# Optimization experiments

Hardware: AMD Instinct MI355X
Metric: run time of the kernel (lower is better)

Reference implementation:

```python
import jax, jax.numpy as jnp
import numpy as np

G_DATA = 262144   # full-resolution grid nodes
G_TRUNC = 40000   # truncated grid nodes
E_EDGES = 1048576 # edges per direction (~4 per data node)
FEAT = 128
EPS = 1e-8


def _sparse_project(x, src, dst, w, dst_size):
    """Row-normalized sparse projection: y[d] = sum_e w_e x[src_e] / sum_e w_e.

    x: [N, G_src, F] -> [N, dst_size, F]
    """
    msg = x[:, src, :] * w[None, :, None]              # [N, E, F] gather-multiply
    out = jnp.zeros((x.shape[0], dst_size, x.shape[2]), dtype=x.dtype)
    out = out.at[:, dst, :].add(msg)                    # scatter-add over dst
    norm = jnp.zeros((dst_size,), dtype=x.dtype).at[dst].add(w)
    return out / jnp.maximum(norm, EPS)[None, :, None]


def setup_inputs() -> dict:
    key = jax.random.key(0)
    ks = jax.random.split(key, 7)
    x = jax.random.normal(ks[0], (1, 2, 1, G_DATA, FEAT), dtype=jnp.float32)
    down_src = jax.random.randint(ks[1], (E_EDGES,), 0, G_DATA, dtype=jnp.int32)
    down_dst = jax.random.randint(ks[2], (E_EDGES,), 0, G_TRUNC, dtype=jnp.int32)
    down_w = jax.random.uniform(ks[3], (E_EDGES,), dtype=jnp.float32)
    up_src = jax.random.randint(ks[4], (E_EDGES,), 0, G_TRUNC, dtype=jnp.int32)
    up_dst = jax.random.randint(ks[5], (E_EDGES,), 0, G_DATA, dtype=jnp.int32)
    up_w = jax.random.uniform(ks[6], (E_EDGES,), dtype=jnp.float32)
    return {"x": x, "down_src": down_src, "down_dst": down_dst, "down_w": down_w,
            "up_src": up_src, "up_dst": up_dst, "up_w": up_w}


def reference(x, down_src, down_dst, down_w, up_src, up_dst, up_w):
    batch = x.shape[0]
    xt = x[:, -1, ...]                                   # [B, E, G, F] take last time step
    b, e, g, f = xt.shape
    xt = xt.reshape(b * e, g, f)                         # (batch ensemble) grid features
    xc = _sparse_project(xt, down_src, down_dst, down_w, G_TRUNC)   # down-project
    xr = _sparse_project(xc, up_src, up_dst, up_w, G_DATA)          # up-project
    return xr.reshape(batch, e, g, f)
```

## Files before the change

kernel.cpp:

```cpp
#include <hip/hip_runtime.h>

#define G_DATA 262144
#define G_TRUNC 40000
#define E_EDGES 1048576
#define FEAT 128
#define EPS 1e-8f


__global__ __launch_bounds__(256) void hist_kernel(const int* __restrict__ dst,
                                                   int* __restrict__ counts) {
    int e = blockIdx.x * 256 + threadIdx.x;
    if (e < E_EDGES) atomicAdd(&counts[dst[e]], 1);
}

__global__ __launch_bounds__(1024) void scan_block(const int* __restrict__ counts,
                                                   int rows,
                                                   int* __restrict__ off,
                                                   int* __restrict__ bsums) {
    __shared__ int s[1024];
    int tid = threadIdx.x;
    int idx = blockIdx.x * 1024 + tid;
    int c = (idx < rows) ? counts[idx] : 0;
    s[tid] = c;
    for (int d = 1; d < 1024; d <<= 1) {
        __syncthreads();
        int t = (tid >= d) ? s[tid - d] : 0;
        __syncthreads();
        s[tid] += t;
    }
    if (idx < rows) off[idx] = s[tid] - c;
    if (tid == 1023) bsums[blockIdx.x] = s[1023];
}

__global__ __launch_bounds__(256) void scan_bsums(int* __restrict__ bsums, int n) {
    __shared__ int s[256];
    int tid = threadIdx.x;
    int v = (tid < n) ? bsums[tid] : 0;
    s[tid] = v;
    for (int d = 1; d < 256; d <<= 1) {
        __syncthreads();
        int t = (tid >= d) ? s[tid - d] : 0;
        __syncthreads();
        s[tid] += t;
    }
    if (tid < n) bsums[tid] = s[tid] - v;
}

__global__ __launch_bounds__(256) void finalize_off(int* __restrict__ off,
                                                    const int* __restrict__ bsums,
                                                    int* __restrict__ cursor,
                                                    int rows, int total) {
    int idx = blockIdx.x * 256 + threadIdx.x;
    if (idx < rows) {
        int o = off[idx] + bsums[idx >> 10];
        off[idx] = o;
        cursor[idx] = o;
    }
    if (idx == 0) off[rows] = total;
}

__global__ __launch_bounds__(256) void scatter_pairs(const int* __restrict__ src,
                                                     const int* __restrict__ dst,
                                                     const float* __restrict__ w,
                                                     int* __restrict__ cursor,
                                                     int2* __restrict__ pairs) {
    int e = blockIdx.x * 256 + threadIdx.x;
    if (e >= E_EDGES) return;
    int d = dst[e];
    int pos = atomicAdd(&cursor[d], 1);
    pairs[pos] = make_int2(src[e], __float_as_int(w[e]));
}

__global__ __launch_bounds__(256) void gather_rows(const float* __restrict__ xsrc,
                                                   const int2* __restrict__ pairs,
                                                   const int* __restrict__ off,
                                                   float* __restrict__ out,
                                                   int rows) {
    long gid = (long)blockIdx.x * 256 + threadIdx.x;
    int r    = (int)(gid >> 6);
    int lane = (int)(gid & 63);
    if (r >= rows) return;
    int beg = off[r], end = off[r + 1];
    float ax = 0.f, ay = 0.f, wsum = 0.f;
    for (int k = beg; k < end; ++k) {
        int2 p = pairs[k];
        float ww = __int_as_float(p.y);
        float2 v = ((const float2*)(xsrc + (size_t)p.x * FEAT))[lane];
        ax += ww * v.x;
        ay += ww * v.y;
        wsum += ww;
    }
    float den = fmaxf(wsum, EPS);
    float2 o;
    o.x = ax / den;
    o.y = ay / den;
    ((float2*)(out + (size_t)r * FEAT))[lane] = o;
}


__global__ __launch_bounds__(256) void norm_accum(const int* __restrict__ dst,
                                                  const float* __restrict__ w,
                                                  float* __restrict__ norm) {
    int i = blockIdx.x * blockDim.x + threadIdx.x;
    if (i < E_EDGES) atomicAdd(&norm[dst[i]], w[i]);
}

__global__ __launch_bounds__(256) void scatter_accum(const float* __restrict__ xsrc,
                                                     const int* __restrict__ src,
                                                     const int* __restrict__ dst,
                                                     const float* __restrict__ w,
                                                     float* __restrict__ out) {
    long gid = (long)blockIdx.x * blockDim.x + threadIdx.x;
    int e    = (int)(gid >> 6);
    int lane = (int)(gid & 63);
    if (e >= E_EDGES) return;
    int   s  = src[e];
    int   d  = dst[e];
    float ww = w[e];
    float2 v = ((const float2*)(xsrc + (size_t)s * FEAT))[lane];
    float* op = out + (size_t)d * FEAT + lane * 2;
    atomicAdd(op,     v.x * ww);
    atomicAdd(op + 1, v.y * ww);
}

__global__ __launch_bounds__(256) void row_divide(float* __restrict__ data,
                                                  const float* __restrict__ norm,
                                                  int rows) {
    long gid = (long)blockIdx.x * blockDim.x + threadIdx.x;
    int r = (int)(gid >> 5);
    int c = (int)(gid & 31);
    if (r >= rows) return;
    float den = fmaxf(norm[r], EPS);
    float4* p = (float4*)(data + (size_t)r * FEAT) + c;
    float4 v = *p;
    v.x /= den; v.y /= den; v.z /= den; v.w /= den;
    *p = v;
}


extern "C" void kernel_launch(void* const* d_in, const int* in_sizes, int n_in,
                              void* d_out, int out_size, void* d_ws, size_t ws_size,
                              hipStream_t stream) {
    const float* x        = (const float*)d_in[0];
    const int*   down_src = (const int*)  d_in[1];
    const int*   down_dst = (const int*)  d_in[2];
    const float* down_w   = (const float*)d_in[3];
    const int*   up_src   = (const int*)  d_in[4];
    const int*   up_dst   = (const int*)  d_in[5];
    const float* up_w     = (const float*)d_in[6];
    float*       out      = (float*)d_out;

    const float* xt = x + (size_t)G_DATA * FEAT;

    const size_t XC_I    = (size_t)G_TRUNC * FEAT;
    const size_t OFF_I   = G_DATA + 2;
    const size_t CUR_I   = G_DATA;
    const size_t CNT_I   = G_DATA;
    const size_t BS_I    = 256;
    const size_t csr_ints = XC_I + OFF_I + CUR_I + CNT_I + BS_I + (size_t)E_EDGES * 2;
    const size_t csr_need = csr_ints * 4;

    if (ws_size >= csr_need) {
        float* xc     = (float*)d_ws;
        int*   off    = (int*)(xc + XC_I);
        int*   cursor = off + OFF_I;
        int*   counts = cursor + CUR_I;
        int*   bsums  = counts + CNT_I;
        int2*  pairs  = (int2*)(bsums + BS_I);

        const int* SRC[2] = { down_src, up_src };
        const int* DST[2] = { down_dst, up_dst };
        const float* WW[2] = { down_w, up_w };
        const float* XS[2] = { xt, xc };
        float* OUT[2] = { xc, out };
        const int ROWS[2] = { G_TRUNC, G_DATA };

        for (int ph = 0; ph < 2; ++ph) {
            int rows = ROWS[ph];
            int nblk = (rows + 1023) / 1024;
            hipMemsetAsync(counts, 0, (size_t)rows * 4, stream);
            hist_kernel<<<E_EDGES / 256, 256, 0, stream>>>(DST[ph], counts);
            scan_block<<<nblk, 1024, 0, stream>>>(counts, rows, off, bsums);
            scan_bsums<<<1, 256, 0, stream>>>(bsums, nblk);
            finalize_off<<<(rows + 255) / 256, 256, 0, stream>>>(off, bsums, cursor, rows, E_EDGES);
            scatter_pairs<<<E_EDGES / 256, 256, 0, stream>>>(SRC[ph], DST[ph], WW[ph], cursor, pairs);
            gather_rows<<<((long)rows * 64 + 255) / 256, 256, 0, stream>>>(XS[ph], pairs, off, OUT[ph], rows);
        }
    } else {
        float* xc        = (float*)d_ws;
        float* norm_down = xc + (size_t)G_TRUNC * FEAT;
        float* norm_up   = norm_down + G_TRUNC;

        size_t ws_need = ((size_t)G_TRUNC * FEAT + G_TRUNC + G_DATA) * sizeof(float);
        size_t ws_zero = ws_need <= ws_size ? ws_need : ws_size;
        hipMemsetAsync(d_ws, 0, ws_zero, stream);
        hipMemsetAsync(d_out, 0, (size_t)out_size * sizeof(float), stream);

        norm_accum<<<E_EDGES / 256, 256, 0, stream>>>(down_dst, down_w, norm_down);
        norm_accum<<<E_EDGES / 256, 256, 0, stream>>>(up_dst,   up_w,   norm_up);
        scatter_accum<<<(E_EDGES * 64) / 256, 256, 0, stream>>>(xt, down_src, down_dst, down_w, xc);
        row_divide<<<(G_TRUNC * 32 + 255) / 256, 256, 0, stream>>>(xc, norm_down, G_TRUNC);
        scatter_accum<<<(E_EDGES * 64) / 256, 256, 0, stream>>>(xc, up_src, up_dst, up_w, out);
        row_divide<<<(G_DATA * 32 + 255) / 256, 256, 0, stream>>>(out, norm_up, G_DATA);
    }
}
```

Baseline: 816.4 us.

## Build both CSR graphs in one pass and unroll gather loops

Merges the down and up edge sets into a single bucket space, so the histogram, scan, offset finalisation and pair scatter run once over both graphs instead of twice. This halves the number of CSR-construction launches. The gather kernel now reads row bounds into scalar registers with readfirstlane and unrolls the edge loop (8 for down, 4 for up) to keep more independent loads in flight. The atomic fallback path is removed, so the code now assumes the workspace is large enough for the combined CSR buffers.

```diff
diff --git a/kernel.cpp b/kernel.cpp
--- a/kernel.cpp
+++ b/kernel.cpp
@@ -5,12 +5,14 @@
 #define E_EDGES 1048576
 #define FEAT 128
 #define EPS 1e-8f
+#define NBUCKET (G_TRUNC + G_DATA)
 
-
-__global__ __launch_bounds__(256) void hist_kernel(const int* __restrict__ dst,
-                                                   int* __restrict__ counts) {
+__global__ __launch_bounds__(256) void hist_fused(const int* __restrict__ down_dst,
+                                                  const int* __restrict__ up_dst,
+                                                  int* __restrict__ counts) {
     int e = blockIdx.x * 256 + threadIdx.x;
-    if (e < E_EDGES) atomicAdd(&counts[dst[e]], 1);
+    if (e < E_EDGES)            atomicAdd(&counts[down_dst[e]], 1);
+    else                        atomicAdd(&counts[G_TRUNC + up_dst[e - E_EDGES]], 1);
 }
 
 __global__ __launch_bounds__(1024) void scan_block(const int* __restrict__ counts,
@@ -32,12 +34,12 @@
     if (tid == 1023) bsums[blockIdx.x] = s[1023];
 }
 
-__global__ __launch_bounds__(256) void scan_bsums(int* __restrict__ bsums, int n) {
-    __shared__ int s[256];
+__global__ __launch_bounds__(512) void scan_bsums(int* __restrict__ bsums, int n) {
+    __shared__ int s[512];
     int tid = threadIdx.x;
     int v = (tid < n) ? bsums[tid] : 0;
     s[tid] = v;
-    for (int d = 1; d < 256; d <<= 1) {
+    for (int d = 1; d < 512; d <<= 1) {
         __syncthreads();
         int t = (tid >= d) ? s[tid - d] : 0;
         __syncthreads();
@@ -59,30 +61,57 @@
     if (idx == 0) off[rows] = total;
 }
 
-__global__ __launch_bounds__(256) void scatter_pairs(const int* __restrict__ src,
-                                                     const int* __restrict__ dst,
-                                                     const float* __restrict__ w,
+__global__ __launch_bounds__(256) void scatter_fused(const int* __restrict__ down_src,
+                                                     const int* __restrict__ down_dst,
+                                                     const float* __restrict__ down_w,
+                                                     const int* __restrict__ up_src,
+                                                     const int* __restrict__ up_dst,
+                                                     const float* __restrict__ up_w,
                                                      int* __restrict__ cursor,
                                                      int2* __restrict__ pairs) {
     int e = blockIdx.x * 256 + threadIdx.x;
-    if (e >= E_EDGES) return;
-    int d = dst[e];
-    int pos = atomicAdd(&cursor[d], 1);
-    pairs[pos] = make_int2(src[e], __float_as_int(w[e]));
+    int b, s; float ww;
+    if (e < E_EDGES) {
+        b = down_dst[e];            s = down_src[e];            ww = down_w[e];
+    } else {
+        int e2 = e - E_EDGES;
+        b = G_TRUNC + up_dst[e2];   s = up_src[e2];             ww = up_w[e2];
+    }
+    int pos = atomicAdd(&cursor[b], 1);
+    pairs[pos] = make_int2(s, __float_as_int(ww));
 }
 
+template<int U>
 __global__ __launch_bounds__(256) void gather_rows(const float* __restrict__ xsrc,
                                                    const int2* __restrict__ pairs,
                                                    const int* __restrict__ off,
                                                    float* __restrict__ out,
-                                                   int rows) {
+                                                   int rows, int row_base) {
     long gid = (long)blockIdx.x * 256 + threadIdx.x;
     int r    = (int)(gid >> 6);
     int lane = (int)(gid & 63);
     if (r >= rows) return;
-    int beg = off[r], end = off[r + 1];
+    int beg = __builtin_amdgcn_readfirstlane(off[row_base + r]);
+    int end = __builtin_amdgcn_readfirstlane(off[row_base + r + 1]);
     float ax = 0.f, ay = 0.f, wsum = 0.f;
-    for (int k = beg; k < end; ++k) {
+    int k = beg;
+    for (; k + U <= end; k += U) {
+        int2 p[U];
+        #pragma unroll
+        for (int u = 0; u < U; ++u) p[u] = pairs[k + u];
+        float2 v[U];
+        #pragma unroll
+        for (int u = 0; u < U; ++u)
+            v[u] = ((const float2*)(xsrc + (size_t)p[u].x * FEAT))[lane];
+        #pragma unroll
+        for (int u = 0; u < U; ++u) {
+            float ww = __int_as_float(p[u].y);
+            ax += ww * v[u].x;
+            ay += ww * v[u].y;
+            wsum += ww;
+        }
+    }
+    for (; k < end; ++k) {
         int2 p = pairs[k];
         float ww = __int_as_float(p.y);
         float2 v = ((const float2*)(xsrc + (size_t)p.x * FEAT))[lane];
@@ -96,47 +125,6 @@
     o.y = ay / den;
     ((float2*)(out + (size_t)r * FEAT))[lane] = o;
 }
-
-
-__global__ __launch_bounds__(256) void norm_accum(const int* __restrict__ dst,
-                                                  const float* __restrict__ w,
-                                                  float* __restrict__ norm) {
-    int i = blockIdx.x * blockDim.x + threadIdx.x;
-    if (i < E_EDGES) atomicAdd(&norm[dst[i]], w[i]);
-}
-
-__global__ __launch_bounds__(256) void scatter_accum(const float* __restrict__ xsrc,
-                                                     const int* __restrict__ src,
-                                                     const int* __restrict__ dst,
-                                                     const float* __restrict__ w,
-                                                     float* __restrict__ out) {
-    long gid = (long)blockIdx.x * blockDim.x + threadIdx.x;
-    int e    = (int)(gid >> 6);
-    int lane = (int)(gid & 63);
-    if (e >= E_EDGES) return;
-    int   s  = src[e];
-    int   d  = dst[e];
-    float ww = w[e];
-    float2 v = ((const float2*)(xsrc + (size_t)s * FEAT))[lane];
-    float* op = out + (size_t)d * FEAT + lane * 2;
-    atomicAdd(op,     v.x * ww);
-    atomicAdd(op + 1, v.y * ww);
-}
-
-__global__ __launch_bounds__(256) void row_divide(float* __restrict__ data,
-                                                  const float* __restrict__ norm,
-                                                  int rows) {
-    long gid = (long)blockIdx.x * blockDim.x + threadIdx.x;
-    int r = (int)(gid >> 5);
-    int c = (int)(gid & 31);
-    if (r >= rows) return;
-    float den = fmaxf(norm[r], EPS);
-    float4* p = (float4*)(data + (size_t)r * FEAT) + c;
-    float4 v = *p;
-    v.x /= den; v.y /= den; v.z /= den; v.w /= den;
-    *p = v;
-}
-
 
 extern "C" void kernel_launch(void* const* d_in, const int* in_sizes, int n_in,
                               void* d_out, int out_size, void* d_ws, size_t ws_size,
@@ -152,55 +140,31 @@
 
     const float* xt = x + (size_t)G_DATA * FEAT;
 
-    const size_t XC_I    = (size_t)G_TRUNC * FEAT;
-    const size_t OFF_I   = G_DATA + 2;
-    const size_t CUR_I   = G_DATA;
-    const size_t CNT_I   = G_DATA;
-    const size_t BS_I    = 256;
-    const size_t csr_ints = XC_I + OFF_I + CUR_I + CNT_I + BS_I + (size_t)E_EDGES * 2;
-    const size_t csr_need = csr_ints * 4;
+    const size_t XC_I  = (size_t)G_TRUNC * FEAT;
+    const size_t CNT_I = NBUCKET;
+    const size_t OFF_I = NBUCKET + 2;
+    const size_t CUR_I = NBUCKET;
+    const size_t BS_I  = 512;
 
-    if (ws_size >= csr_need) {
-        float* xc     = (float*)d_ws;
-        int*   off    = (int*)(xc + XC_I);
-        int*   cursor = off + OFF_I;
-        int*   counts = cursor + CUR_I;
-        int*   bsums  = counts + CNT_I;
-        int2*  pairs  = (int2*)(bsums + BS_I);
+    float* xc     = (float*)d_ws;
+    int*   counts = (int*)(xc + XC_I);
+    int*   off    = counts + CNT_I;
+    int*   cursor = off + OFF_I;
+    int*   bsums  = cursor + CUR_I;
+    int2*  pairs  = (int2*)(bsums + BS_I);
 
-        const int* SRC[2] = { down_src, up_src };
-        const int* DST[2] = { down_dst, up_dst };
-        const float* WW[2] = { down_w, up_w };
-        const float* XS[2] = { xt, xc };
-        float* OUT[2] = { xc, out };
-        const int ROWS[2] = { G_TRUNC, G_DATA };
+    const int TOTAL_E = 2 * E_EDGES;
+    const int nblk = (NBUCKET + 1023) / 1024;
 
-        for (int ph = 0; ph < 2; ++ph) {
-            int rows = ROWS[ph];
-            int nblk = (rows + 1023) / 1024;
-            hipMemsetAsync(counts, 0, (size_t)rows * 4, stream);
-            hist_kernel<<<E_EDGES / 256, 256, 0, stream>>>(DST[ph], counts);
-            scan_block<<<nblk, 1024, 0, stream>>>(counts, rows, off, bsums);
-            scan_bsums<<<1, 256, 0, stream>>>(bsums, nblk);
-            finalize_off<<<(rows + 255) / 256, 256, 0, stream>>>(off, bsums, cursor, rows, E_EDGES);
-            scatter_pairs<<<E_EDGES / 256, 256, 0, stream>>>(SRC[ph], DST[ph], WW[ph], cursor, pairs);
-            gather_rows<<<((long)rows * 64 + 255) / 256, 256, 0, stream>>>(XS[ph], pairs, off, OUT[ph], rows);
-        }
-    } else {
-        float* xc        = (float*)d_ws;
-        float* norm_down = xc + (size_t)G_TRUNC * FEAT;
-        float* norm_up   = norm_down + G_TRUNC;
-
-        size_t ws_need = ((size_t)G_TRUNC * FEAT + G_TRUNC + G_DATA) * sizeof(float);
-        size_t ws_zero = ws_need <= ws_size ? ws_need : ws_size;
-        hipMemsetAsync(d_ws, 0, ws_zero, stream);
-        hipMemsetAsync(d_out, 0, (size_t)out_size * sizeof(float), stream);
-
-        norm_accum<<<E_EDGES / 256, 256, 0, stream>>>(down_dst, down_w, norm_down);
-        norm_accum<<<E_EDGES / 256, 256, 0, stream>>>(up_dst,   up_w,   norm_up);
-        scatter_accum<<<(E_EDGES * 64) / 256, 256, 0, stream>>>(xt, down_src, down_dst, down_w, xc);
-        row_divide<<<(G_TRUNC * 32 + 255) / 256, 256, 0, stream>>>(xc, norm_down, G_TRUNC);
-        scatter_accum<<<(E_EDGES * 64) / 256, 256, 0, stream>>>(xc, up_src, up_dst, up_w, out);
-        row_divide<<<(G_DATA * 32 + 255) / 256, 256, 0, stream>>>(out, norm_up, G_DATA);
-    }
+    hipMemsetAsync(counts, 0, (size_t)NBUCKET * 4, stream);
+    hist_fused<<<TOTAL_E / 256, 256, 0, stream>>>(down_dst, up_dst, counts);
+    scan_block<<<nblk, 1024, 0, stream>>>(counts, NBUCKET, off, bsums);
+    scan_bsums<<<1, 512, 0, stream>>>(bsums, nblk);
+    finalize_off<<<(NBUCKET + 255) / 256, 256, 0, stream>>>(off, bsums, cursor, NBUCKET, TOTAL_E);
+    scatter_fused<<<TOTAL_E / 256, 256, 0, stream>>>(down_src, down_dst, down_w,
+                                                     up_src, up_dst, up_w, cursor, pairs);
+    gather_rows<8><<<((long)G_TRUNC * 64 + 255) / 256, 256, 0, stream>>>(
+        xt, pairs, off, xc, G_TRUNC, 0);
+    gather_rows<4><<<((long)G_DATA * 64 + 255) / 256, 256, 0, stream>>>(
+        xc, pairs, off, out, G_DATA, G_TRUNC);
 }
```

Measured after the change: 734.1 us. 10.1% less time.
